# Kernel tuning notes

Hardware: AMD Instinct MI355X
Metric: run time of the kernel (lower is better)

The kernel has to match this reference:

```python
import jax, jax.numpy as jnp
import numpy as np
from jax import lax

DN3D = ('NDHWC', 'DHWIO', 'NDHWC')


def _conv3d(x, w):
    return lax.conv_general_dilated(x, w, window_strides=(1, 1, 1),
                                    padding='VALID', dimension_numbers=DN3D)


def _cconv3d(xr, xi, wr, wi):
    # (xr + i xi) * (wr + i wi)
    yr = _conv3d(xr, wr) - _conv3d(xi, wi)
    yi = _conv3d(xr, wi) + _conv3d(xi, wr)
    return yr, yi


def _project(wr, wi, zero_mean):
    # zero-mean + bound-norm weight projection over (kD,kH,kW,Cin) per output filter
    ax = (0, 1, 2, 3)
    if zero_mean:
        wr = wr - jnp.mean(wr, ax, keepdims=True)
        wi = wi - jnp.mean(wi, ax, keepdims=True)
    norm = jnp.sqrt(jnp.sum(wr * wr + wi * wi, ax, keepdims=True))
    s = 1.0 / jnp.maximum(norm, 1.0)
    return wr * s, wi * s


def _sympad(x, pads):
    # pads: list of (lo, hi) per axis
    return jnp.pad(x, pads, mode='symmetric')


def setup_inputs() -> dict:
    key = jax.random.key(0)
    ks = jax.random.split(key, 6)
    B, T, Z, Y, X, C = 2, 8, 20, 64, 64, 2
    F1, F = 32, 32
    return {
        'xr': jax.random.normal(ks[0], (B, T, Z, Y, X, C), jnp.float32),
        'xi': jax.random.normal(ks[1], (B, T, Z, Y, X, C), jnp.float32),
        'wxyz_r': jax.random.normal(ks[2], (3, 3, 3, C, F1), jnp.float32) * 0.1,
        'wxyz_i': jax.random.normal(ks[3], (3, 3, 3, C, F1), jnp.float32) * 0.1,
        'wt_r': jax.random.normal(ks[4], (3, 1, 1, F1, F), jnp.float32) * 0.1,
        'wt_i': jax.random.normal(ks[5], (3, 1, 1, F1, F), jnp.float32) * 0.1,
    }


def reference(xr, xi, wxyz_r, wxyz_i, wt_r, wt_i):
    B, T, Z, Y, X, C = xr.shape
    kz, ky, kx = wxyz_r.shape[0], wxyz_r.shape[1], wxyz_r.shape[2]
    kt = wt_r.shape[0]
    F1 = wxyz_r.shape[-1]
    F = wt_r.shape[-1]

    # projected (zero-mean, bound-norm) complex kernels
    wsr, wsi = _project(wxyz_r, wxyz_i, zero_mean=True)
    wtr, wti = _project(wt_r, wt_i, zero_mean=False)

    # --- spatial 3D conv over (Z,Y,X): fold T into batch (== per-T-slice loop)
    sr = xr.reshape(B * T, Z, Y, X, C)
    si = xi.reshape(B * T, Z, Y, X, C)
    pads_sp = [(0, 0), (kz // 2, kz // 2), (ky // 2, ky // 2), (kx // 2, kx // 2), (0, 0)]
    sr = _sympad(sr, pads_sp)
    si = _sympad(si, pads_sp)
    spr, spi = _cconv3d(sr, si, wsr, wsi)          # [B*T, Z, Y, X, F1]
    spr = spr.reshape(B, T, Z, Y, X, F1)
    spi = spi.reshape(B, T, Z, Y, X, F1)

    # --- temporal conv (kt,1,1) over (T,Z,Y): fold X into batch (== per-X-slice loop)
    tr = spr.transpose(0, 4, 1, 2, 3, 5).reshape(B * X, T, Z, Y, F1)
    ti = spi.transpose(0, 4, 1, 2, 3, 5).reshape(B * X, T, Z, Y, F1)
    pads_t = [(0, 0), (kt // 2, kt // 2), (0, 0), (0, 0), (0, 0)]
    tr = _sympad(tr, pads_t)
    ti = _sympad(ti, pads_t)
    ytr, yti = _cconv3d(tr, ti, wtr, wti)          # [B*X, T, Z, Y, F]
    yr = ytr.reshape(B, X, T, Z, Y, F).transpose(0, 2, 3, 4, 1, 5)
    yi = yti.reshape(B, X, T, Z, Y, F).transpose(0, 2, 3, 4, 1, 5)
    return yr, yi
```

## Files before the change

kernel.cpp:

```cpp
#include <hip/hip_runtime.h>

#define B_ 2
#define T_ 8
#define Z_ 20
#define Y_ 64
#define X_ 64
#define C_ 2
#define F1_ 32
#define F_ 32

constexpr int NPTS = B_*T_*Z_*Y_*X_;
constexpr int ZYX  = Z_*Y_*X_;

constexpr int RING_STRIDE = 36;
constexpr int SLOT_DW     = 16*RING_STRIDE;
constexpr int HALO        = 3*3*18;

using bf8   = __attribute__((ext_vector_type(8))) short;
using f32x4 = __attribute__((ext_vector_type(4))) float;

__device__ inline unsigned short f2bf(float x) {
    unsigned u = __builtin_bit_cast(unsigned, x);
    return (unsigned short)((u + 0x7fff + ((u >> 16) & 1)) >> 16);
}
__device__ inline unsigned pk(float a, float b) {
    return (unsigned)f2bf(a) | ((unsigned)f2bf(b) << 16);
}

__global__ __launch_bounds__(64) void project_kernel(
    const float* __restrict__ wxr, const float* __restrict__ wxi,
    const float* __restrict__ wtr, const float* __restrict__ wti,
    float* __restrict__ psr, float* __restrict__ psi,
    float* __restrict__ otr, float* __restrict__ oti)
{
    const int bid  = blockIdx.x;
    const int lane = threadIdx.x;

    if (bid < F1_) {
        const int f = bid;
        float er = 0.f, ei = 0.f;
        if (lane < 54) { er = wxr[lane*F1_ + f]; ei = wxi[lane*F1_ + f]; }
        float sr = er, si = ei;
        #pragma unroll
        for (int o = 32; o >= 1; o >>= 1) { sr += __shfl_xor(sr, o); si += __shfl_xor(si, o); }
        const float mr = sr * (1.f/54.f), mi = si * (1.f/54.f);
        const float dr = er - mr, di = ei - mi;
        float sq = (lane < 54) ? (dr*dr + di*di) : 0.f;
        #pragma unroll
        for (int o = 32; o >= 1; o >>= 1) sq += __shfl_xor(sq, o);
        const float s = 1.f / fmaxf(sqrtf(sq), 1.f);
        if (lane < 54) { psr[lane*F1_ + f] = dr*s; psi[lane*F1_ + f] = di*s; }
    } else {
        const int f = bid - F1_;
        float er[2], ei[2];
        float sq = 0.f;
        #pragma unroll
        for (int k = 0; k < 2; ++k) {
            const int e = lane + k*64;
            if (e < 96) { er[k] = wtr[e*F_ + f]; ei[k] = wti[e*F_ + f]; sq += er[k]*er[k] + ei[k]*ei[k]; }
            else        { er[k] = 0.f;  ei[k] = 0.f; }
        }
        #pragma unroll
        for (int o = 32; o >= 1; o >>= 1) sq += __shfl_xor(sq, o);
        const float s = 1.f / fmaxf(sqrtf(sq), 1.f);
        #pragma unroll
        for (int k = 0; k < 2; ++k) {
            const int e = lane + k*64;
            if (e < 96) { otr[e*F_ + f] = er[k]*s; oti[e*F_ + f] = ei[k]*s; }
        }
    }
}

__global__ __launch_bounds__(256) void pack_kernel(
    const float* __restrict__ psr, const float* __restrict__ psi,
    const float* __restrict__ ptr_, const float* __restrict__ pti,
    unsigned short* __restrict__ wsp, unsigned short* __restrict__ wp)
{
    const int g = blockIdx.x;
    if (g < 16) {
        for (int o = g*512 + threadIdx.x; o < (g+1)*512; o += 256) {
            const int j  = o & 7;
            const int l  = (o >> 3) & 63;
            const int gg = o >> 9;
            const int kb = gg & 3, ct = gg >> 2;
            const int k  = kb*32 + (l >> 4)*8 + j;
            const int n  = ct*16 + (l & 15);
            float v = 0.f;
            if (k < 108) {
                const int tap = k >> 2, q = k & 3, cin = q & 1, cp = q >> 1;
                const int f  = n & 31;
                const float wr = psr[(tap*2 + cin)*F1_ + f];
                const float wi = psi[(tap*2 + cin)*F1_ + f];
                v = (n < 32) ? (cp ? -wi : wr) : (cp ? wr : wi);
            }
            wsp[o] = f2bf(v);
        }
    } else {
        for (int o = (g-16)*512 + threadIdx.x; o < (g-15)*512; o += 256) {
            const int j  = o & 7;
            const int l  = (o >> 3) & 63;
            const int gg = o >> 9;
            const int kb = gg % 6, ct = gg / 6;
            const int k  = kb*32 + (l >> 4)*8 + j;
            const int n  = ct*16 + (l & 15);
            const int kt = k >> 6, f1 = (k >> 1) & 31, c = k & 1;
            const int f  = n & 31;
            const float wr = ptr_[(kt*F1_ + f1)*F_ + f];
            const float wi = pti[(kt*F1_ + f1)*F_ + f];
            const float v  = (n < 32) ? (c ? -wi : wr) : (c ? wr : wi);
            wp[o] = f2bf(v);
        }
    }
}

__global__ __launch_bounds__(256) void repack_kernel(
    const float* __restrict__ xr, const float* __restrict__ xi,
    uint2* __restrict__ xb)
{
    const int p = blockIdx.x*256 + threadIdx.x;
    const float2 vr = *reinterpret_cast<const float2*>(xr + (size_t)p*2);
    const float2 vi = *reinterpret_cast<const float2*>(xi + (size_t)p*2);
    uint2 v;
    v.x = (unsigned)f2bf(vr.x) | ((unsigned)f2bf(vr.y) << 16);
    v.y = (unsigned)f2bf(vi.x) | ((unsigned)f2bf(vi.y) << 16);
    xb[p] = v;
}

__global__ __launch_bounds__(256, 2) void fused_kernel(
    const uint2* __restrict__ xb,
    const unsigned short* __restrict__ wsp,
    const unsigned short* __restrict__ wp,
    float* __restrict__ yr, float* __restrict__ yi)
{
    __shared__ uint4 ring4[4*3*SLOT_DW/4];
    __shared__ uint2 slab[4][2][HALO];
    unsigned* ring = reinterpret_cast<unsigned*>(ring4);

    const int tid  = threadIdx.x;
    const int lane = tid & 63;
    const int wid  = tid >> 6;
    const int lx   = lane & 15;
    const int lg   = lane >> 4;

    const int bq = blockIdx.x;
    const int y  = bq & 63;
    const int z  = (bq >> 6) % Z_;
    const int b  = bq / (64*Z_);
    const int x0 = wid * 16;

    bf8 wsf[4][4];
    const bf8* w8 = reinterpret_cast<const bf8*>(wsp);
    #pragma unroll
    for (int ct = 0; ct < 4; ++ct)
        #pragma unroll
        for (int kb = 0; kb < 4; ++kb)
            wsf[ct][kb] = w8[(ct*4 + kb)*64 + lane];

    bf8 wtf[4][6];
    const bf8* wp8 = reinterpret_cast<const bf8*>(wp);
    #pragma unroll
    for (int ct = 0; ct < 4; ++ct)
        #pragma unroll
        for (int kb = 0; kb < 6; ++kb)
            wtf[ct][kb] = wp8[(ct*6 + kb)*64 + lane];

    int xoff[3];
    #pragma unroll
    for (int i = 0; i < 3; ++i) {
        int it = lane + i*64; if (it >= HALO) it = HALO-1;
        const int iz = it / 54;
        const int iy = (it / 18) % 3;
        const int ix = it % 18;
        int zz = z + iz - 1;  zz = zz < 0 ? 0 : (zz >= Z_ ? Z_-1 : zz);
        int yy = y + iy - 1;  yy = yy < 0 ? 0 : (yy >= Y_ ? Y_-1 : yy);
        int xx = x0 + ix - 1; xx = xx < 0 ? 0 : (xx >= X_ ? X_-1 : xx);
        xoff[i] = (zz*Y_ + yy)*X_ + xx;
    }

    int o8[4][2];
    #pragma unroll
    for (int kb = 0; kb < 4; ++kb)
        #pragma unroll
        for (int s = 0; s < 2; ++s) {
            int ta = kb*8 + lg*2 + s; if (ta > 26) ta = 26;
            const int dz = ta/9, dyx = ta - dz*9, dy = dyx/3, dx = dyx - dy*3;
            o8[kb][s] = (dz*3 + dy)*18 + dx + lx;
        }

    unsigned* myring  = ring + wid*3*SLOT_DW;
    const int  rbase  = lx*RING_STRIDE + lg*4;
    const size_t orow = (((size_t)b*T_)*Z_ + z)*(size_t)(Y_*X_) + (size_t)y*X_ + x0 + lx;

    uint4 cur_lo, cur_hi;
    uint2 stmp[3];

    auto STAGE_ISSUE = [&](int t) {
        const uint2* xt = xb + (size_t)(b*T_ + t)*ZYX;
        stmp[0] = xt[xoff[0]];
        stmp[1] = xt[xoff[1]];
        if (lane < HALO - 128) stmp[2] = xt[xoff[2]];
    };
    auto STAGE_WRITE = [&](int bufsel) {
        uint2* s = slab[wid][bufsel];
        s[lane]      = stmp[0];
        s[lane + 64] = stmp[1];
        if (lane < HALO - 128) s[lane + 128] = stmp[2];
    };

    auto SPATIAL = [&](int bufsel) {
        const uint2* s = slab[wid][bufsel];
        bf8 af[4];
        #pragma unroll
        for (int kb = 0; kb < 4; ++kb) {
            const uint2 lo = s[o8[kb][0]];
            const uint2 hi = s[o8[kb][1]];
            af[kb] = __builtin_bit_cast(bf8, make_uint4(lo.x, lo.y, hi.x, hi.y));
        }
        f32x4 acc[4];
        #pragma unroll
        for (int ct = 0; ct < 4; ++ct) acc[ct] = (f32x4){0.f,0.f,0.f,0.f};
        #pragma unroll
        for (int ct = 0; ct < 4; ++ct)
            #pragma unroll
            for (int kb = 0; kb < 4; ++kb)
                acc[ct] = __builtin_amdgcn_mfma_f32_16x16x32_bf16(
                              wsf[ct][kb], af[kb], acc[ct], 0, 0, 0);
        cur_lo = make_uint4(pk(acc[0][0],acc[2][0]), pk(acc[0][1],acc[2][1]),
                            pk(acc[0][2],acc[2][2]), pk(acc[0][3],acc[2][3]));
        cur_hi = make_uint4(pk(acc[1][0],acc[3][0]), pk(acc[1][1],acc[3][1]),
                            pk(acc[1][2],acc[3][2]), pk(acc[1][3],acc[3][3]));
    };

    auto WRITE = [&](int t) {
        unsigned* s = myring + (t % 3)*SLOT_DW + rbase;
        *reinterpret_cast<uint4*>(s)      = cur_lo;
        *reinterpret_cast<uint4*>(s + 16) = cur_hi;
    };

    auto EMIT = [&](int sa, int sb, int tout) {
        const unsigned* pa = myring + (sa % 3)*SLOT_DW + rbase;
        const unsigned* pb = myring + (sb % 3)*SLOT_DW + rbase;
        bf8 fr[6];
        fr[0] = __builtin_bit_cast(bf8, *reinterpret_cast<const uint4*>(pa));
        fr[1] = __builtin_bit_cast(bf8, *reinterpret_cast<const uint4*>(pa + 16));
        fr[2] = __builtin_bit_cast(bf8, *reinterpret_cast<const uint4*>(pb));
        fr[3] = __builtin_bit_cast(bf8, *reinterpret_cast<const uint4*>(pb + 16));
        fr[4] = __builtin_bit_cast(bf8, cur_lo);
        fr[5] = __builtin_bit_cast(bf8, cur_hi);
        f32x4 acc[4];
        #pragma unroll
        for (int ct = 0; ct < 4; ++ct) acc[ct] = (f32x4){0.f,0.f,0.f,0.f};
        #pragma unroll
        for (int ct = 0; ct < 4; ++ct)
            #pragma unroll
            for (int kb = 0; kb < 6; ++kb)
                acc[ct] = __builtin_amdgcn_mfma_f32_16x16x32_bf16(
                              wtf[ct][kb], fr[kb], acc[ct], 0, 0, 0);
        const size_t p = orow + (size_t)tout * ZYX;
        #pragma unroll
        for (int ct = 0; ct < 4; ++ct) {
            float* outp = (ct < 2) ? yr : yi;
            *reinterpret_cast<f32x4*>(outp + p*F_ + (ct & 1)*16 + lg*4) = acc[ct];
        }
    };

    STAGE_ISSUE(0);
    STAGE_WRITE(0);
    STAGE_ISSUE(1);
    SPATIAL(0);
    WRITE(0);

    #pragma unroll 1
    for (int t = 1; t < T_; ++t) {
        STAGE_WRITE(t & 1);
        if (t < T_-1) STAGE_ISSUE(t+1);
        SPATIAL(t & 1);
        EMIT(t-2 < 0 ? 0 : t-2, t-1, t-1);
        WRITE(t);
    }
    EMIT(T_-2, T_-1, T_-1);
}

extern "C" void kernel_launch(void* const* d_in, const int* in_sizes, int n_in,
                              void* d_out, int out_size, void* d_ws, size_t ws_size,
                              hipStream_t stream)
{
    const float* xr  = (const float*)d_in[0];
    const float* xi  = (const float*)d_in[1];
    const float* wxr = (const float*)d_in[2];
    const float* wxi = (const float*)d_in[3];
    const float* wtr = (const float*)d_in[4];
    const float* wti = (const float*)d_in[5];

    float* ws   = (float*)d_ws;
    float* psr  = ws;
    float* psi  = ws + 2048;
    float* ptr_ = ws + 4096;
    float* pti  = ws + 8192;
    unsigned short* wsp = (unsigned short*)(ws + 12288);
    unsigned short* wp  = (unsigned short*)(ws + 16384);
    uint2* xb           = (uint2*)(ws + 32768);

    float* yr = (float*)d_out;
    float* yi = yr + (size_t)NPTS * F_;

    hipLaunchKernelGGL(project_kernel, dim3(64), dim3(64), 0, stream,
                       wxr, wxi, wtr, wti, psr, psi, ptr_, pti);
    hipLaunchKernelGGL(pack_kernel, dim3(40), dim3(256), 0, stream,
                       psr, psi, ptr_, pti, wsp, wp);
    hipLaunchKernelGGL(repack_kernel, dim3(NPTS/256), dim3(256), 0, stream,
                       xr, xi, xb);
    hipLaunchKernelGGL(fused_kernel, dim3(B_*Z_*Y_), dim3(256), 0, stream,
                       xb, wsp, wp, yr, yi);
}
```

Baseline: 97.54 us.

## Process two 16-wide x tiles per wave to share halo staging

Each wave now covers 32 x positions instead of 16, and each block covers two y rows instead of one, which halves the grid. The halo slab grows to 34 columns, so the x-overlap loads are shared between two adjacent 16-column MFMA tiles, and each wave keeps two temporal ring buffers. This reduces the redundant halo loads per output and the number of blocks. In exchange it doubles the ring LDS and live registers per wave, which may lower occupancy below the requested 2 blocks per CU.

```diff
diff --git a/kernel.cpp b/kernel.cpp
--- a/kernel.cpp
+++ b/kernel.cpp
@@ -14,7 +14,7 @@
 
 constexpr int RING_STRIDE = 36;
 constexpr int SLOT_DW     = 16*RING_STRIDE;
-constexpr int HALO        = 3*3*18;
+constexpr int HALO2       = 3*3*34;
 
 using bf8   = __attribute__((ext_vector_type(8))) short;
 using f32x4 = __attribute__((ext_vector_type(4))) float;
@@ -132,8 +132,8 @@
     const unsigned short* __restrict__ wp,
     float* __restrict__ yr, float* __restrict__ yi)
 {
-    __shared__ uint4 ring4[4*3*SLOT_DW/4];
-    __shared__ uint2 slab[4][2][HALO];
+    __shared__ uint4 ring4[4*2*3*SLOT_DW/4];
+    __shared__ uint2 slab[4][2][HALO2];
     unsigned* ring = reinterpret_cast<unsigned*>(ring4);
 
     const int tid  = threadIdx.x;
@@ -142,11 +142,12 @@
     const int lx   = lane & 15;
     const int lg   = lane >> 4;
 
-    const int bq = blockIdx.x;
-    const int y  = bq & 63;
-    const int z  = (bq >> 6) % Z_;
-    const int b  = bq / (64*Z_);
-    const int x0 = wid * 16;
+    const int bq    = blockIdx.x;
+    const int ypair = bq & 31;
+    const int z     = (bq >> 5) % Z_;
+    const int b     = bq / (32*Z_);
+    const int y     = ypair*2 + (wid >> 1);
+    const int x0    = (wid & 1) * 32;
 
     bf8 wsf[4][4];
     const bf8* w8 = reinterpret_cast<const bf8*>(wsp);
@@ -164,13 +165,13 @@
         for (int kb = 0; kb < 6; ++kb)
             wtf[ct][kb] = wp8[(ct*6 + kb)*64 + lane];
 
-    int xoff[3];
+    int xoff[5];
     #pragma unroll
-    for (int i = 0; i < 3; ++i) {
-        int it = lane + i*64; if (it >= HALO) it = HALO-1;
-        const int iz = it / 54;
-        const int iy = (it / 18) % 3;
-        const int ix = it % 18;
+    for (int i = 0; i < 5; ++i) {
+        int it = lane + i*64; if (it >= HALO2) it = HALO2-1;
+        const int iz = it / 102;
+        const int iy = (it / 34) % 3;
+        const int ix = it % 34;
         int zz = z + iz - 1;  zz = zz < 0 ? 0 : (zz >= Z_ ? Z_-1 : zz);
         int yy = y + iy - 1;  yy = yy < 0 ? 0 : (yy >= Y_ ? Y_-1 : yy);
         int xx = x0 + ix - 1; xx = xx < 0 ? 0 : (xx >= X_ ? X_-1 : xx);
@@ -184,37 +185,37 @@
         for (int s = 0; s < 2; ++s) {
             int ta = kb*8 + lg*2 + s; if (ta > 26) ta = 26;
             const int dz = ta/9, dyx = ta - dz*9, dy = dyx/3, dx = dyx - dy*3;
-            o8[kb][s] = (dz*3 + dy)*18 + dx + lx;
-        }
-
-    unsigned* myring  = ring + wid*3*SLOT_DW;
+            o8[kb][s] = (dz*3 + dy)*34 + dx + lx;
+        }
+
+    unsigned* myring  = ring + wid*(2*3*SLOT_DW);
     const int  rbase  = lx*RING_STRIDE + lg*4;
     const size_t orow = (((size_t)b*T_)*Z_ + z)*(size_t)(Y_*X_) + (size_t)y*X_ + x0 + lx;
 
-    uint4 cur_lo, cur_hi;
-    uint2 stmp[3];
+    uint4 caLo, caHi, cbLo, cbHi;
+    uint2 stmp[5];
 
     auto STAGE_ISSUE = [&](int t) {
         const uint2* xt = xb + (size_t)(b*T_ + t)*ZYX;
-        stmp[0] = xt[xoff[0]];
-        stmp[1] = xt[xoff[1]];
-        if (lane < HALO - 128) stmp[2] = xt[xoff[2]];
+        #pragma unroll
+        for (int i = 0; i < 4; ++i) stmp[i] = xt[xoff[i]];
+        if (lane < HALO2 - 256) stmp[4] = xt[xoff[4]];
     };
     auto STAGE_WRITE = [&](int bufsel) {
         uint2* s = slab[wid][bufsel];
-        s[lane]      = stmp[0];
-        s[lane + 64] = stmp[1];
-        if (lane < HALO - 128) s[lane + 128] = stmp[2];
-    };
-
-    auto SPATIAL = [&](int bufsel) {
+        #pragma unroll
+        for (int i = 0; i < 4; ++i) s[lane + i*64] = stmp[i];
+        if (lane < HALO2 - 256) s[lane + 256] = stmp[4];
+    };
+
+    auto SPATIAL = [&](int bufsel, int xadd, uint4& lo, uint4& hi) {
         const uint2* s = slab[wid][bufsel];
         bf8 af[4];
         #pragma unroll
         for (int kb = 0; kb < 4; ++kb) {
-            const uint2 lo = s[o8[kb][0]];
-            const uint2 hi = s[o8[kb][1]];
-            af[kb] = __builtin_bit_cast(bf8, make_uint4(lo.x, lo.y, hi.x, hi.y));
+            const uint2 l2 = s[o8[kb][0] + xadd];
+            const uint2 h2 = s[o8[kb][1] + xadd];
+            af[kb] = __builtin_bit_cast(bf8, make_uint4(l2.x, l2.y, h2.x, h2.y));
         }
         f32x4 acc[4];
         #pragma unroll
@@ -225,28 +226,30 @@
             for (int kb = 0; kb < 4; ++kb)
                 acc[ct] = __builtin_amdgcn_mfma_f32_16x16x32_bf16(
                               wsf[ct][kb], af[kb], acc[ct], 0, 0, 0);
-        cur_lo = make_uint4(pk(acc[0][0],acc[2][0]), pk(acc[0][1],acc[2][1]),
-                            pk(acc[0][2],acc[2][2]), pk(acc[0][3],acc[2][3]));
-        cur_hi = make_uint4(pk(acc[1][0],acc[3][0]), pk(acc[1][1],acc[3][1]),
-                            pk(acc[1][2],acc[3][2]), pk(acc[1][3],acc[3][3]));
-    };
-
-    auto WRITE = [&](int t) {
-        unsigned* s = myring + (t % 3)*SLOT_DW + rbase;
-        *reinterpret_cast<uint4*>(s)      = cur_lo;
-        *reinterpret_cast<uint4*>(s + 16) = cur_hi;
-    };
-
-    auto EMIT = [&](int sa, int sb, int tout) {
-        const unsigned* pa = myring + (sa % 3)*SLOT_DW + rbase;
-        const unsigned* pb = myring + (sb % 3)*SLOT_DW + rbase;
+        lo = make_uint4(pk(acc[0][0],acc[2][0]), pk(acc[0][1],acc[2][1]),
+                        pk(acc[0][2],acc[2][2]), pk(acc[0][3],acc[2][3]));
+        hi = make_uint4(pk(acc[1][0],acc[3][0]), pk(acc[1][1],acc[3][1]),
+                        pk(acc[1][2],acc[3][2]), pk(acc[1][3],acc[3][3]));
+    };
+
+    auto WRITE = [&](int tsel, int t, const uint4& lo, const uint4& hi) {
+        unsigned* s = myring + tsel*(3*SLOT_DW) + (t % 3)*SLOT_DW + rbase;
+        *reinterpret_cast<uint4*>(s)      = lo;
+        *reinterpret_cast<uint4*>(s + 16) = hi;
+    };
+
+    auto EMIT = [&](int tsel, const uint4& clo, const uint4& chi,
+                    int sa, int sb, int tout) {
+        const unsigned* tb = myring + tsel*(3*SLOT_DW);
+        const unsigned* pa = tb + (sa % 3)*SLOT_DW + rbase;
+        const unsigned* pb = tb + (sb % 3)*SLOT_DW + rbase;
         bf8 fr[6];
         fr[0] = __builtin_bit_cast(bf8, *reinterpret_cast<const uint4*>(pa));
         fr[1] = __builtin_bit_cast(bf8, *reinterpret_cast<const uint4*>(pa + 16));
         fr[2] = __builtin_bit_cast(bf8, *reinterpret_cast<const uint4*>(pb));
         fr[3] = __builtin_bit_cast(bf8, *reinterpret_cast<const uint4*>(pb + 16));
-        fr[4] = __builtin_bit_cast(bf8, cur_lo);
-        fr[5] = __builtin_bit_cast(bf8, cur_hi);
+        fr[4] = __builtin_bit_cast(bf8, clo);
+        fr[5] = __builtin_bit_cast(bf8, chi);
         f32x4 acc[4];
         #pragma unroll
         for (int ct = 0; ct < 4; ++ct) acc[ct] = (f32x4){0.f,0.f,0.f,0.f};
@@ -256,7 +259,7 @@
             for (int kb = 0; kb < 6; ++kb)
                 acc[ct] = __builtin_amdgcn_mfma_f32_16x16x32_bf16(
                               wtf[ct][kb], fr[kb], acc[ct], 0, 0, 0);
-        const size_t p = orow + (size_t)tout * ZYX;
+        const size_t p = orow + tsel*16 + (size_t)tout * ZYX;
         #pragma unroll
         for (int ct = 0; ct < 4; ++ct) {
             float* outp = (ct < 2) ? yr : yi;
@@ -267,18 +270,25 @@
     STAGE_ISSUE(0);
     STAGE_WRITE(0);
     STAGE_ISSUE(1);
-    SPATIAL(0);
-    WRITE(0);
+    SPATIAL(0, 0,  caLo, caHi);
+    SPATIAL(0, 16, cbLo, cbHi);
+    WRITE(0, 0, caLo, caHi);
+    WRITE(1, 0, cbLo, cbHi);
 
     #pragma unroll 1
     for (int t = 1; t < T_; ++t) {
         STAGE_WRITE(t & 1);
         if (t < T_-1) STAGE_ISSUE(t+1);
-        SPATIAL(t & 1);
-        EMIT(t-2 < 0 ? 0 : t-2, t-1, t-1);
-        WRITE(t);
+        const int sa = t-2 < 0 ? 0 : t-2;
+        SPATIAL(t & 1, 0,  caLo, caHi);
+        SPATIAL(t & 1, 16, cbLo, cbHi);
+        EMIT(0, caLo, caHi, sa, t-1, t-1);
+        EMIT(1, cbLo, cbHi, sa, t-1, t-1);
+        WRITE(0, t, caLo, caHi);
+        WRITE(1, t, cbLo, cbHi);
     }
-    EMIT(T_-2, T_-1, T_-1);
+    EMIT(0, caLo, caHi, T_-2, T_-1, T_-1);
+    EMIT(1, cbLo, cbHi, T_-2, T_-1, T_-1);
 }
 
 extern "C" void kernel_launch(void* const* d_in, const int* in_sizes, int n_in,
@@ -310,6 +320,6 @@
                        psr, psi, ptr_, pti, wsp, wp);
     hipLaunchKernelGGL(repack_kernel, dim3(NPTS/256), dim3(256), 0, stream,
                        xr, xi, xb);
-    hipLaunchKernelGGL(fused_kernel, dim3(B_*Z_*Y_), dim3(256), 0, stream,
+    hipLaunchKernelGGL(fused_kernel, dim3(B_*Z_*(Y_/2)), dim3(256), 0, stream,
                        xb, wsp, wp, yr, yi);
 }
```

Result: faster. 91.91 us (-5.8%).
